# Performance work log

Measured on AMD Instinct MI355X. Metric: run time of the kernel, lower is better.

The kernel has to match this reference:

```python
import jax, jax.numpy as jnp
import numpy as np

B, H, W, C = 8, 224, 224, 96
WS, SS, NH = 7, 3, 3  # window size, shift size, num heads
HD = C // NH
N = WS * WS
nW = (H // WS) * (W // WS)


def _rel_pos_index():
    coords = np.stack(np.meshgrid(np.arange(WS), np.arange(WS), indexing='ij'))  # (2,WS,WS)
    flat = coords.reshape(2, -1)
    rel = (flat[:, :, None] - flat[:, None, :]).transpose(1, 2, 0)  # (N,N,2)
    rel[:, :, 0] += WS - 1
    rel[:, :, 1] += WS - 1
    rel[:, :, 0] *= 2 * WS - 1
    return jnp.asarray(rel.sum(-1))  # (N,N) int


def _shift_mask():
    img = np.zeros((H, W), np.int32)
    cnt = 0
    sls = (slice(0, -WS), slice(-WS, -SS), slice(-SS, None))
    for hs in sls:
        for ws_ in sls:
            img[hs, ws_] = cnt
            cnt += 1
    m = img.reshape(H // WS, WS, W // WS, WS).transpose(0, 2, 1, 3).reshape(-1, N)  # (nW,N)
    diff = m[:, :, None] - m[:, None, :]
    return jnp.asarray(np.where(diff != 0, -100.0, 0.0).astype(np.float32))  # (nW,N,N)


def setup_inputs() -> dict:
    key = jax.random.key(0)
    ks = jax.random.split(key, 10)
    s = 0.02
    return {
        'x': jax.random.normal(ks[0], (B, H * W, C), jnp.float32),
        'mask': _shift_mask(),
        'norm1_g': jnp.ones((C,), jnp.float32),
        'norm1_b': jnp.zeros((C,), jnp.float32),
        'qkv_w': s * jax.random.normal(ks[1], (3 * C, C), jnp.float32),
        'qkv_b': jnp.zeros((3 * C,), jnp.float32),
        'rpb_table': s * jax.random.normal(ks[2], ((2 * WS - 1) * (2 * WS - 1), NH), jnp.float32),
        'proj_w': s * jax.random.normal(ks[3], (C, C), jnp.float32),
        'proj_b': jnp.zeros((C,), jnp.float32),
        'norm2_g': jnp.ones((C,), jnp.float32),
        'norm2_b': jnp.zeros((C,), jnp.float32),
        'fc1_w': s * jax.random.normal(ks[4], (4 * C, C), jnp.float32),
        'fc1_b': jnp.zeros((4 * C,), jnp.float32),
        'fc2_w': s * jax.random.normal(ks[5], (C, 4 * C), jnp.float32),
        'fc2_b': jnp.zeros((C,), jnp.float32),
    }


def _ln(x, g, b):
    mu = x.mean(-1, keepdims=True)
    var = x.var(-1, keepdims=True)
    return (x - mu) * jax.lax.rsqrt(var + 1e-5) * g + b


def _win_partition(x):  # (B,H,W,C) -> (B*nW, N, C)
    x = x.reshape(B, H // WS, WS, W // WS, WS, C)
    return x.transpose(0, 1, 3, 2, 4, 5).reshape(-1, N, C)


def _win_reverse(w):  # (B*nW, N, C) -> (B,H,W,C)
    w = w.reshape(B, H // WS, W // WS, WS, WS, C)
    return w.transpose(0, 1, 3, 2, 4, 5).reshape(B, H, W, C)


def reference(x, mask, norm1_g, norm1_b, qkv_w, qkv_b, rpb_table, proj_w, proj_b,
              norm2_g, norm2_b, fc1_w, fc1_b, fc2_w, fc2_b):
    rel_idx = _rel_pos_index()  # (N,N) constant
    shortcut = x
    h = _ln(x, norm1_g, norm1_b).reshape(B, H, W, C)
    h = jnp.roll(h, shift=(-SS, -SS), axis=(1, 2))  # cyclic shift
    xw = _win_partition(h)  # (B*nW, N, C)
    B_ = xw.shape[0]
    qkv = (xw @ qkv_w.T + qkv_b).reshape(B_, N, 3, NH, HD).transpose(2, 0, 3, 1, 4)
    q, k, v = qkv[0], qkv[1], qkv[2]  # (B_,NH,N,HD)
    scale = HD ** -0.5
    attn = jnp.einsum('bhid,bhjd->bhij', q * scale, k)  # (B_,NH,N,N)
    bias = rpb_table[rel_idx.reshape(-1)].reshape(N, N, NH).transpose(2, 0, 1)  # (NH,N,N)
    attn = attn + bias[None]
    attn = attn.reshape(B, nW, NH, N, N) + mask[None, :, None]
    attn = jax.nn.softmax(attn.reshape(B_, NH, N, N), axis=-1)
    out = jnp.einsum('bhij,bhjd->bhid', attn, v).transpose(0, 2, 1, 3).reshape(B_, N, C)
    out = out @ proj_w.T + proj_b
    h = _win_reverse(out)
    h = jnp.roll(h, shift=(SS, SS), axis=(1, 2)).reshape(B, H * W, C)
    x = shortcut + h
    # MLP
    m = _ln(x, norm2_g, norm2_b)
    m = jax.nn.gelu(m @ fc1_w.T + fc1_b, approximate=False)
    m = m @ fc2_w.T + fc2_b
    return x + m
```

## Files before the change

### kernel.cpp

```cpp
#include <hip/hip_runtime.h>
#include <hip/hip_bf16.h>
#include <stdint.h>

typedef __attribute__((ext_vector_type(4))) float f32x4;
typedef __bf16 bfv8 __attribute__((ext_vector_type(8)));
typedef unsigned short u16x8 __attribute__((ext_vector_type(8)));
typedef unsigned short u16x4 __attribute__((ext_vector_type(4)));

#define DEV static __device__ __forceinline__

DEV float b2f(unsigned short h) {
    unsigned u = ((unsigned)h) << 16;
    return __builtin_bit_cast(float, u);
}
DEV unsigned short f2b(float f) {
    unsigned u = __builtin_bit_cast(unsigned, f);
    u += 0x7fffu + ((u >> 16) & 1u);
    return (unsigned short)(u >> 16);
}
DEV unsigned short f2bn(float f) {
    return __builtin_bit_cast(unsigned short, (__bf16)f);
}
DEV bfv8 ldb8(const unsigned short* p) {
    return __builtin_bit_cast(bfv8, *(const u16x8*)p);
}
DEV void stb4(unsigned short* p, f32x4 v) {
    u16x4 o;
    o[0] = f2bn(v[0]); o[1] = f2bn(v[1]); o[2] = f2bn(v[2]); o[3] = f2bn(v[3]);
    *(u16x4*)p = o;
}

static constexpr int T = 401408;

__global__ __launch_bounds__(256) void k_prep(const float* __restrict__ qkvw,
                                              const float* __restrict__ projw,
                                              const float* __restrict__ w1,
                                              const float* __restrict__ w2,
                                              const float* __restrict__ rpb,
                                              const float* __restrict__ mask,
                                              unsigned short* __restrict__ wb,
                                              float* __restrict__ cmb) {
    int i = blockIdx.x * 256 + threadIdx.x;
    if (i < 110592) {
        float v;
        if (i < 27648) v = qkvw[i];
        else if (i < 36864) v = projw[i - 27648];
        else if (i < 73728) v = w1[i - 36864];
        else v = w2[i - 73728];
        wb[i] = f2b(v);
    } else if (i < 110592 + 49152) {
        int j = i - 110592;
        int t = j / 12288, rem = j - t * 12288;
        int h = rem >> 12, nm = rem & 4095;
        int n = nm >> 6, m = nm & 63;
        float v = -10000.f;
        if (n < 49 && m < 49) {
            int i1 = n / 7, j1 = n - i1 * 7, i2 = m / 7, j2 = m - i2 * 7;
            int rel = (i1 - i2 + 6) * 13 + (j1 - j2 + 6);
            int rep = ((t & 1) ? 31 : 0) + ((t & 2) ? 992 : 0);
            v = rpb[rel * 3 + h] + mask[rep * 2401 + n * 49 + m];
        }
        cmb[j] = v;
    }
}

__global__ __launch_bounds__(192) void k_attnf(const float* __restrict__ x,
                                               const float* __restrict__ g1,
                                               const float* __restrict__ be1,
                                               const unsigned short* __restrict__ qkvwb,
                                               const float* __restrict__ qkvb,
                                               const float* __restrict__ cmb,
                                               unsigned short* __restrict__ aout) {
    __shared__ unsigned short smem[10368 + 3 * 5120];
    unsigned short* xs = smem;

    unsigned win = blockIdx.x;
    unsigned b = win >> 10, widx = win & 1023u;
    unsigned wi = widx >> 5, wj = widx & 31u;
    int tid = threadIdx.x, wv = tid >> 6, lane = tid & 63;
    int half = lane >> 5, lch = lane & 31;

    for (int it = 0; it < 9; ++it) {
        int tok = it * 6 + wv * 2 + half;
        if (tok < 49) {
            unsigned i = (unsigned)tok / 7u, j = (unsigned)tok - i * 7u;
            unsigned sr = wi * 7 + i + 3; if (sr >= 224) sr -= 224;
            unsigned sc = wj * 7 + j + 3; if (sc >= 224) sc -= 224;
            const float* src = x + (size_t)(b * 50176u + sr * 224u + sc) * 96;
            float v0 = src[lch], v1 = src[lch + 32], v2 = src[lch + 64];
            float s = v0 + v1 + v2, q = v0 * v0 + v1 * v1 + v2 * v2;
#pragma unroll
            for (int off = 1; off < 32; off <<= 1) {
                s += __shfl_xor(s, off);
                q += __shfl_xor(q, off);
            }
            float mu = s * (1.f / 96.f);
            float rstd = rsqrtf(q * (1.f / 96.f) - mu * mu + 1e-5f);
            xs[tok * 104 + lch]      = f2bn((v0 - mu) * rstd * g1[lch] + be1[lch]);
            xs[tok * 104 + lch + 32] = f2bn((v1 - mu) * rstd * g1[lch + 32] + be1[lch + 32]);
            xs[tok * 104 + lch + 64] = f2bn((v2 - mu) * rstd * g1[lch + 64] + be1[lch + 64]);
        }
    }
    for (int t = tid; t < 15 * 96; t += 192)
        xs[(49 + t / 96) * 104 + (t % 96)] = 0;
    __syncthreads();

    int h = wv;
    int rlo = lane & 15, g4 = lane >> 4;
    bfv8 a[4][3];
#pragma unroll
    for (int mt = 0; mt < 4; ++mt)
#pragma unroll
        for (int ks = 0; ks < 3; ++ks)
            a[mt][ks] = ldb8(xs + (mt * 16 + rlo) * 104 + ks * 32 + g4 * 8);
    __syncthreads();

    unsigned short* vtH = smem + h * 3456;
    unsigned short* qH  = smem + 10368 + h * 5120;
    unsigned short* kH  = qH + 2560;
    unsigned short* pH  = qH;

    const float SC = 0.17677669529663687f;
    int colbase[6] = {32 * h, 32 * h + 16, 96 + 32 * h, 96 + 32 * h + 16,
                      192 + 32 * h, 192 + 32 * h + 16};
#pragma unroll
    for (int grp = 0; grp < 2; ++grp) {
        bfv8 wS[3][3];
        f32x4 bS[3];
#pragma unroll
        for (int q3 = 0; q3 < 3; ++q3) {
            int c = colbase[grp * 3 + q3] + rlo;
            wS[q3][0] = ldb8(qkvwb + (size_t)c * 96 + g4 * 8);
            wS[q3][1] = ldb8(qkvwb + (size_t)c * 96 + 32 + g4 * 8);
            wS[q3][2] = ldb8(qkvwb + (size_t)c * 96 + 64 + g4 * 8);
            bS[q3] = *(const f32x4*)(qkvb + colbase[grp * 3 + q3] + g4 * 4);
        }
#pragma unroll
        for (int q3 = 0; q3 < 3; ++q3) {
            int nt = grp * 3 + q3;
#pragma unroll
            for (int mt = 0; mt < 4; ++mt) {
                f32x4 acc = {0.f, 0.f, 0.f, 0.f};
                acc = __builtin_amdgcn_mfma_f32_16x16x32_bf16(wS[q3][0], a[mt][0], acc, 0, 0, 0);
                acc = __builtin_amdgcn_mfma_f32_16x16x32_bf16(wS[q3][1], a[mt][1], acc, 0, 0, 0);
                acc = __builtin_amdgcn_mfma_f32_16x16x32_bf16(wS[q3][2], a[mt][2], acc, 0, 0, 0);
                int token = mt * 16 + rlo;
                if (nt < 2) {
                    f32x4 v = (acc + bS[q3]) * SC;
                    stb4(qH + token * 40 + nt * 16 + g4 * 4, v);
                } else if (nt < 4) {
                    f32x4 v = acc + bS[q3];
                    stb4(kH + token * 40 + (nt - 2) * 16 + g4 * 4, v);
                } else {
#pragma unroll
                    for (int r = 0; r < 4; ++r)
                        vtH[((nt - 4) * 16 + g4 * 4 + r) * 72 + token] =
                            f2bn(acc[r] + bS[q3][r]);
                }
            }
        }
    }
    vtH[32 * 72 + lane] = 0x3F80;

    bfv8 qf[4], kf[4];
#pragma unroll
    for (int t = 0; t < 4; ++t) {
        qf[t] = ldb8(qH + (t * 16 + rlo) * 40 + g4 * 8);
        kf[t] = ldb8(kH + (t * 16 + rlo) * 40 + g4 * 8);
    }
    f32x4 s[4][4];
#pragma unroll
    for (int mt = 0; mt < 4; ++mt)
#pragma unroll
        for (int nt = 0; nt < 4; ++nt) {
            f32x4 acc0 = {0.f, 0.f, 0.f, 0.f};
            s[mt][nt] = __builtin_amdgcn_mfma_f32_16x16x32_bf16(kf[nt], qf[mt], acc0, 0, 0, 0);
        }
    int type = ((wi == 31) ? 2 : 0) | ((wj == 31) ? 1 : 0);
    const float* crow = cmb + ((size_t)(type * 3 + h) << 12);
#pragma unroll
    for (int mt = 0; mt < 4; ++mt) {
        int query = mt * 16 + rlo;
        const float* cr = crow + query * 64;
#pragma unroll
        for (int nt = 0; nt < 4; ++nt) {
            f32x4 cv = *(const f32x4*)(cr + nt * 16 + g4 * 4);
            f32x4 p;
#pragma unroll
            for (int r = 0; r < 4; ++r) p[r] = __expf(s[mt][nt][r] + cv[r]);
            stb4(pH + query * 72 + nt * 16 + g4 * 4, p);
        }
    }
    bfv8 vf[2][3];
#pragma unroll
    for (int ks = 0; ks < 2; ++ks)
#pragma unroll
        for (int db = 0; db < 3; ++db)
            vf[ks][db] = ldb8(vtH + (db * 16 + rlo) * 72 + ks * 32 + g4 * 8);
#pragma unroll
    for (int mt = 0; mt < 4; ++mt) {
        bfv8 pa0 = ldb8(pH + (mt * 16 + rlo) * 72 + g4 * 8);
        bfv8 pa1 = ldb8(pH + (mt * 16 + rlo) * 72 + 32 + g4 * 8);
        f32x4 acc[3];
#pragma unroll
        for (int db = 0; db < 3; ++db) {
            acc[db] = {0.f, 0.f, 0.f, 0.f};
            acc[db] = __builtin_amdgcn_mfma_f32_16x16x32_bf16(vf[0][db], pa0, acc[db], 0, 0, 0);
            acc[db] = __builtin_amdgcn_mfma_f32_16x16x32_bf16(vf[1][db], pa1, acc[db], 0, 0, 0);
        }
        float inv = 1.f / __shfl(acc[2][0], rlo);
        int query = mt * 16 + rlo;
        if (query < 49) {
            unsigned short* ob = aout + ((size_t)win * 49 + query) * 96 + h * 32;
#pragma unroll
            for (int db = 0; db < 2; ++db) {
                f32x4 v = acc[db] * inv;
                stb4(ob + db * 16 + g4 * 4, v);
            }
        }
    }
}

__global__ __launch_bounds__(128, 3) void k_pm(const unsigned short* __restrict__ aout,
                                               const unsigned short* __restrict__ projwb,
                                               const float* __restrict__ projb,
                                               const float* __restrict__ x,
                                               const float* __restrict__ g2,
                                               const float* __restrict__ be2,
                                               const unsigned short* __restrict__ w1b,
                                               const float* __restrict__ bias1,
                                               const unsigned short* __restrict__ w2b,
                                               const float* __restrict__ bias2,
                                               float* __restrict__ out) {
    __shared__ unsigned short smem[2 * 32 * 204];
    int lane = threadIdx.x & 63, wv = threadIdx.x >> 6;
    int rlo = lane & 15, g4 = lane >> 4;
    size_t tok0 = (size_t)blockIdx.x * 64;
    unsigned short* mw = smem + wv * 6528;

    bfv8 a0[2][3];
    int pix[2];
#pragma unroll
    for (int t = 0; t < 2; ++t) {
        int tt = 2 * wv + t;
        const unsigned short* p = aout + (tok0 + tt * 16 + rlo) * 96 + g4 * 8;
        a0[t][0] = ldb8(p); a0[t][1] = ldb8(p + 32); a0[t][2] = ldb8(p + 64);
        unsigned wt = (unsigned)(tok0 + tt * 16 + rlo);
        unsigned win = wt / 49u, n = wt - win * 49u;
        unsigned b = win >> 10, widx = win & 1023u;
        unsigned wi = widx >> 5, wj = widx & 31u;
        unsigned i = n / 7u, j = n - i * 7u;
        unsigned sr = wi * 7 + i + 3; if (sr >= 224) sr -= 224;
        unsigned sc = wj * 7 + j + 3; if (sc >= 224) sc -= 224;
        pix[t] = (int)(b * 50176u + sr * 224u + sc);
    }

    f32x4 xv[2][6];
    float rs[2] = {0.f, 0.f}, rq[2] = {0.f, 0.f};
#pragma unroll
    for (int nt = 0; nt < 6; ++nt) {
        int c = nt * 16 + rlo;
        bfv8 b0 = ldb8(projwb + (size_t)c * 96 + g4 * 8);
        bfv8 b1 = ldb8(projwb + (size_t)c * 96 + 32 + g4 * 8);
        bfv8 b2 = ldb8(projwb + (size_t)c * 96 + 64 + g4 * 8);
        f32x4 bv = *(const f32x4*)(projb + nt * 16 + g4 * 4);
#pragma unroll
        for (int t = 0; t < 2; ++t) {
            f32x4 acc = {0.f, 0.f, 0.f, 0.f};
            acc = __builtin_amdgcn_mfma_f32_16x16x32_bf16(b0, a0[t][0], acc, 0, 0, 0);
            acc = __builtin_amdgcn_mfma_f32_16x16x32_bf16(b1, a0[t][1], acc, 0, 0, 0);
            acc = __builtin_amdgcn_mfma_f32_16x16x32_bf16(b2, a0[t][2], acc, 0, 0, 0);
            f32x4 xr = *(const f32x4*)(x + (size_t)pix[t] * 96 + nt * 16 + g4 * 4);
            f32x4 v = acc + bv + xr;
            xv[t][nt] = v;
            rs[t] += v[0] + v[1] + v[2] + v[3];
            rq[t] += v[0] * v[0] + v[1] * v[1] + v[2] * v[2] + v[3] * v[3];
        }
    }
#pragma unroll
    for (int t = 0; t < 2; ++t) {
        float s = rs[t], q = rq[t];
        s += __shfl_xor(s, 16); q += __shfl_xor(q, 16);
        s += __shfl_xor(s, 32); q += __shfl_xor(q, 32);
        float mu = s * (1.f / 96.f);
        float rstd = rsqrtf(q * (1.f / 96.f) - mu * mu + 1e-5f);
#pragma unroll
        for (int nt = 0; nt < 6; ++nt) {
            f32x4 gg = *(const f32x4*)(g2 + nt * 16 + g4 * 4);
            f32x4 bb = *(const f32x4*)(be2 + nt * 16 + g4 * 4);
            f32x4 v;
#pragma unroll
            for (int r = 0; r < 4; ++r) v[r] = (xv[t][nt][r] - mu) * rstd * gg[r] + bb[r];
            stb4(mw + (t * 16 + rlo) * 104 + nt * 16 + g4 * 4, v);
        }
    }
    bfv8 af[2][3];
#pragma unroll
    for (int mt = 0; mt < 2; ++mt)
#pragma unroll
        for (int ks = 0; ks < 3; ++ks)
            af[mt][ks] = ldb8(mw + (mt * 16 + rlo) * 104 + ks * 32 + g4 * 8);

    f32x4 acc2[2][6];
#pragma unroll
    for (int t = 0; t < 2; ++t)
#pragma unroll
        for (int nt = 0; nt < 6; ++nt) acc2[t][nt] = {0.f, 0.f, 0.f, 0.f};

#pragma unroll
    for (int half = 0; half < 2; ++half) {
#pragma unroll
        for (int ct = 0; ct < 12; ++ct) {
            int cb = half * 192 + ct * 16;
            int c = cb + rlo;
            bfv8 b0 = ldb8(w1b + (size_t)c * 96 + g4 * 8);
            bfv8 b1 = ldb8(w1b + (size_t)c * 96 + 32 + g4 * 8);
            bfv8 b2 = ldb8(w1b + (size_t)c * 96 + 64 + g4 * 8);
            f32x4 bv = *(const f32x4*)(bias1 + cb + g4 * 4);
#pragma unroll
            for (int mt = 0; mt < 2; ++mt) {
                f32x4 acc = {0.f, 0.f, 0.f, 0.f};
                acc = __builtin_amdgcn_mfma_f32_16x16x32_bf16(b0, af[mt][0], acc, 0, 0, 0);
                acc = __builtin_amdgcn_mfma_f32_16x16x32_bf16(b1, af[mt][1], acc, 0, 0, 0);
                acc = __builtin_amdgcn_mfma_f32_16x16x32_bf16(b2, af[mt][2], acc, 0, 0, 0);
                f32x4 g;
#pragma unroll
                for (int r = 0; r < 4; ++r) {
                    float v = acc[r] + bv[r];
                    float z = 1.5957691216057308f * (v + 0.044715f * v * v * v);
                    g[r] = v / (1.f + __expf(-z));
                }
                stb4(mw + (mt * 16 + rlo) * 204 + ct * 16 + g4 * 4, g);
            }
        }
#pragma unroll
        for (int ks = 0; ks < 6; ++ks) {
            bfv8 am0 = ldb8(mw + (0 * 16 + rlo) * 204 + ks * 32 + g4 * 8);
            bfv8 am1 = ldb8(mw + (1 * 16 + rlo) * 204 + ks * 32 + g4 * 8);
#pragma unroll
            for (int nt = 0; nt < 6; ++nt) {
                bfv8 bw = ldb8(w2b + (size_t)(nt * 16 + rlo) * 384 + half * 192 + ks * 32 + g4 * 8);
                acc2[0][nt] = __builtin_amdgcn_mfma_f32_16x16x32_bf16(bw, am0, acc2[0][nt], 0, 0, 0);
                acc2[1][nt] = __builtin_amdgcn_mfma_f32_16x16x32_bf16(bw, am1, acc2[1][nt], 0, 0, 0);
            }
        }
    }

#pragma unroll
    for (int t = 0; t < 2; ++t)
#pragma unroll
        for (int nt = 0; nt < 6; ++nt) {
            f32x4 bv = *(const f32x4*)(bias2 + nt * 16 + g4 * 4);
            f32x4 ov = acc2[t][nt] + bv + xv[t][nt];
            *(f32x4*)(out + (size_t)pix[t] * 96 + nt * 16 + g4 * 4) = ov;
        }
}

extern "C" void kernel_launch(void* const* d_in, const int* in_sizes, int n_in,
                              void* d_out, int out_size, void* d_ws, size_t ws_size,
                              hipStream_t stream) {
    const float* x     = (const float*)d_in[0];
    const float* mask  = (const float*)d_in[1];
    const float* n1g   = (const float*)d_in[2];
    const float* n1b   = (const float*)d_in[3];
    const float* qkvw  = (const float*)d_in[4];
    const float* qkvb  = (const float*)d_in[5];
    const float* rpb   = (const float*)d_in[6];
    const float* projw = (const float*)d_in[7];
    const float* projb = (const float*)d_in[8];
    const float* n2g   = (const float*)d_in[9];
    const float* n2b   = (const float*)d_in[10];
    const float* fc1w  = (const float*)d_in[11];
    const float* fc1b  = (const float*)d_in[12];
    const float* fc2w  = (const float*)d_in[13];
    const float* fc2b  = (const float*)d_in[14];

    if (ws_size < 77488128ULL) return;
    char* ws = (char*)d_ws;
    unsigned short* aout = (unsigned short*)ws;
    unsigned short* wb   = (unsigned short*)(ws + 77070336);
    float*          cmb  = (float*)(ws + 77291520);
    float*          out  = (float*)d_out;

    unsigned short* qkvwb  = wb;
    unsigned short* projwb = wb + 27648;
    unsigned short* fc1wb  = wb + 36864;
    unsigned short* fc2wb  = wb + 73728;

    k_prep<<<624, 256, 0, stream>>>(qkvw, projw, fc1w, fc2w, rpb, mask, wb, cmb);
    k_attnf<<<8192, 192, 0, stream>>>(x, n1g, n1b, qkvwb, qkvb, cmb, aout);
    k_pm<<<T / 64, 128, 0, stream>>>(aout, projwb, projb, x, n2g, n2b,
                                     fc1wb, fc1b, fc2wb, fc2b, out);
}
```

Measured before the change: 455.1 us.

## Normalize softmax before PV and shrink MLP hidden chunks to cut LDS

```diff
diff --git a/kernel.cpp b/kernel.cpp
--- a/kernel.cpp
+++ b/kernel.cpp
@@ -71,7 +71,7 @@
                                                const float* __restrict__ qkvb,
                                                const float* __restrict__ cmb,
                                                unsigned short* __restrict__ aout) {
-    __shared__ unsigned short smem[10368 + 3 * 5120];
+    __shared__ unsigned short smem[6912 + 3 * 5120];
     unsigned short* xs = smem;
 
     unsigned win = blockIdx.x;
@@ -115,8 +115,8 @@
             a[mt][ks] = ldb8(xs + (mt * 16 + rlo) * 104 + ks * 32 + g4 * 8);
     __syncthreads();
 
-    unsigned short* vtH = smem + h * 3456;
-    unsigned short* qH  = smem + 10368 + h * 5120;
+    unsigned short* vtH = smem + h * 2304;
+    unsigned short* qH  = smem + 6912 + h * 5120;
     unsigned short* kH  = qH + 2560;
     unsigned short* pH  = qH;
 
@@ -160,7 +160,6 @@
             }
         }
     }
-    vtH[32 * 72 + lane] = 0x3F80;
 
     bfv8 qf[4], kf[4];
 #pragma unroll
@@ -182,46 +181,49 @@
     for (int mt = 0; mt < 4; ++mt) {
         int query = mt * 16 + rlo;
         const float* cr = crow + query * 64;
+        float rsum = 0.f;
 #pragma unroll
         for (int nt = 0; nt < 4; ++nt) {
             f32x4 cv = *(const f32x4*)(cr + nt * 16 + g4 * 4);
-            f32x4 p;
-#pragma unroll
-            for (int r = 0; r < 4; ++r) p[r] = __expf(s[mt][nt][r] + cv[r]);
-            stb4(pH + query * 72 + nt * 16 + g4 * 4, p);
-        }
-    }
-    bfv8 vf[2][3];
+#pragma unroll
+            for (int r = 0; r < 4; ++r) {
+                float p = __expf(s[mt][nt][r] + cv[r]);
+                s[mt][nt][r] = p;
+                rsum += p;
+            }
+        }
+        rsum += __shfl_xor(rsum, 16);
+        rsum += __shfl_xor(rsum, 32);
+        float inv = 1.f / rsum;
+#pragma unroll
+        for (int nt = 0; nt < 4; ++nt) {
+            f32x4 v = s[mt][nt] * inv;
+            stb4(pH + query * 72 + nt * 16 + g4 * 4, v);
+        }
+    }
+    bfv8 vf[2][2];
 #pragma unroll
     for (int ks = 0; ks < 2; ++ks)
 #pragma unroll
-        for (int db = 0; db < 3; ++db)
+        for (int db = 0; db < 2; ++db)
             vf[ks][db] = ldb8(vtH + (db * 16 + rlo) * 72 + ks * 32 + g4 * 8);
 #pragma unroll
     for (int mt = 0; mt < 4; ++mt) {
         bfv8 pa0 = ldb8(pH + (mt * 16 + rlo) * 72 + g4 * 8);
         bfv8 pa1 = ldb8(pH + (mt * 16 + rlo) * 72 + 32 + g4 * 8);
-        f32x4 acc[3];
-#pragma unroll
-        for (int db = 0; db < 3; ++db) {
-            acc[db] = {0.f, 0.f, 0.f, 0.f};
-            acc[db] = __builtin_amdgcn_mfma_f32_16x16x32_bf16(vf[0][db], pa0, acc[db], 0, 0, 0);
-            acc[db] = __builtin_amdgcn_mfma_f32_16x16x32_bf16(vf[1][db], pa1, acc[db], 0, 0, 0);
-        }
-        float inv = 1.f / __shfl(acc[2][0], rlo);
         int query = mt * 16 + rlo;
-        if (query < 49) {
-            unsigned short* ob = aout + ((size_t)win * 49 + query) * 96 + h * 32;
-#pragma unroll
-            for (int db = 0; db < 2; ++db) {
-                f32x4 v = acc[db] * inv;
-                stb4(ob + db * 16 + g4 * 4, v);
-            }
-        }
-    }
-}
-
-__global__ __launch_bounds__(128, 3) void k_pm(const unsigned short* __restrict__ aout,
+#pragma unroll
+        for (int db = 0; db < 2; ++db) {
+            f32x4 acc = {0.f, 0.f, 0.f, 0.f};
+            acc = __builtin_amdgcn_mfma_f32_16x16x32_bf16(vf[0][db], pa0, acc, 0, 0, 0);
+            acc = __builtin_amdgcn_mfma_f32_16x16x32_bf16(vf[1][db], pa1, acc, 0, 0, 0);
+            if (query < 49)
+                stb4(aout + ((size_t)win * 49 + query) * 96 + h * 32 + db * 16 + g4 * 4, acc);
+        }
+    }
+}
+
+__global__ __launch_bounds__(128, 4) void k_pm(const unsigned short* __restrict__ aout,
                                                const unsigned short* __restrict__ projwb,
                                                const float* __restrict__ projb,
                                                const float* __restrict__ x,
@@ -232,11 +234,11 @@
                                                const unsigned short* __restrict__ w2b,
                                                const float* __restrict__ bias2,
                                                float* __restrict__ out) {
-    __shared__ unsigned short smem[2 * 32 * 204];
+    __shared__ unsigned short smem[2 * 32 * 136];
     int lane = threadIdx.x & 63, wv = threadIdx.x >> 6;
     int rlo = lane & 15, g4 = lane >> 4;
     size_t tok0 = (size_t)blockIdx.x * 64;
-    unsigned short* mw = smem + wv * 6528;
+    unsigned short* mw = smem + wv * 4352;
 
     bfv8 a0[2][3];
     int pix[2];
@@ -291,7 +293,7 @@
             f32x4 v;
 #pragma unroll
             for (int r = 0; r < 4; ++r) v[r] = (xv[t][nt][r] - mu) * rstd * gg[r] + bb[r];
-            stb4(mw + (t * 16 + rlo) * 104 + nt * 16 + g4 * 4, v);
+            stb4(mw + (t * 16 + rlo) * 136 + nt * 16 + g4 * 4, v);
         }
     }
     bfv8 af[2][3];
@@ -299,7 +301,7 @@
     for (int mt = 0; mt < 2; ++mt)
 #pragma unroll
         for (int ks = 0; ks < 3; ++ks)
-            af[mt][ks] = ldb8(mw + (mt * 16 + rlo) * 104 + ks * 32 + g4 * 8);
+            af[mt][ks] = ldb8(mw + (mt * 16 + rlo) * 136 + ks * 32 + g4 * 8);
 
     f32x4 acc2[2][6];
 #pragma unroll
@@ -308,10 +310,10 @@
         for (int nt = 0; nt < 6; ++nt) acc2[t][nt] = {0.f, 0.f, 0.f, 0.f};
 
 #pragma unroll
-    for (int half = 0; half < 2; ++half) {
-#pragma unroll
-        for (int ct = 0; ct < 12; ++ct) {
-            int cb = half * 192 + ct * 16;
+    for (int ch = 0; ch < 3; ++ch) {
+#pragma unroll
+        for (int ct = 0; ct < 8; ++ct) {
+            int cb = ch * 128 + ct * 16;
             int c = cb + rlo;
             bfv8 b0 = ldb8(w1b + (size_t)c * 96 + g4 * 8);
             bfv8 b1 = ldb8(w1b + (size_t)c * 96 + 32 + g4 * 8);
@@ -330,16 +332,16 @@
                     float z = 1.5957691216057308f * (v + 0.044715f * v * v * v);
                     g[r] = v / (1.f + __expf(-z));
                 }
-                stb4(mw + (mt * 16 + rlo) * 204 + ct * 16 + g4 * 4, g);
-            }
-        }
-#pragma unroll
-        for (int ks = 0; ks < 6; ++ks) {
-            bfv8 am0 = ldb8(mw + (0 * 16 + rlo) * 204 + ks * 32 + g4 * 8);
-            bfv8 am1 = ldb8(mw + (1 * 16 + rlo) * 204 + ks * 32 + g4 * 8);
+                stb4(mw + (mt * 16 + rlo) * 136 + ct * 16 + g4 * 4, g);
+            }
+        }
+#pragma unroll
+        for (int ks = 0; ks < 4; ++ks) {
+            bfv8 am0 = ldb8(mw + (0 * 16 + rlo) * 136 + ks * 32 + g4 * 8);
+            bfv8 am1 = ldb8(mw + (1 * 16 + rlo) * 136 + ks * 32 + g4 * 8);
 #pragma unroll
             for (int nt = 0; nt < 6; ++nt) {
-                bfv8 bw = ldb8(w2b + (size_t)(nt * 16 + rlo) * 384 + half * 192 + ks * 32 + g4 * 8);
+                bfv8 bw = ldb8(w2b + (size_t)(nt * 16 + rlo) * 384 + ch * 128 + ks * 32 + g4 * 8);
                 acc2[0][nt] = __builtin_amdgcn_mfma_f32_16x16x32_bf16(bw, am0, acc2[0][nt], 0, 0, 0);
                 acc2[1][nt] = __builtin_amdgcn_mfma_f32_16x16x32_bf16(bw, am1, acc2[1][nt], 0, 0, 0);
             }
```

After: 530.7 us. 1.17x slower.
